# Kernel tuning notes

Measured on AMD Instinct MI355X. Metric: run time of the kernel, lower is better.

The kernel has to match this reference:

```python
import jax, jax.numpy as jnp
import numpy as np

B, T, C, H = 4, 4096, 1024, 64

def setup_inputs() -> dict:
    key = jax.random.key(0)
    kx, kk, kq, kv = jax.random.split(key, 4)
    x = jax.random.normal(kx, (B, T, C), dtype=jnp.float32)
    # causal lower-triangular mask; masked_fill where mask == 0
    mask = jnp.tril(jnp.ones((T, T), dtype=jnp.int32))
    s = 1.0 / np.sqrt(C)
    Wk = jax.random.normal(kk, (H, C), dtype=jnp.float32) * s
    Wq = jax.random.normal(kq, (H, C), dtype=jnp.float32) * s
    Wv = jax.random.normal(kv, (H, C), dtype=jnp.float32) * s
    return {"x": x, "mask": mask, "Wk": Wk, "Wq": Wq, "Wv": Wv}

def reference(x, mask, Wk, Wq, Wv):
    # single-head attention; dropout is identity in eval mode
    scale = Wk.shape[0] ** -0.5  # head_size ** -0.5
    k = jnp.einsum('btc,hc->bth', x, Wk)  # [B,T,H]
    q = jnp.einsum('btc,hc->bth', x, Wq)
    v = jnp.einsum('btc,hc->bth', x, Wv)
    att = jnp.einsum('bqh,bkh->bqk', q, k) * scale  # [B,T,T]
    att = jnp.where(mask == 0, -jnp.inf, att)
    att = jax.nn.softmax(att, axis=-1)
    out = jnp.einsum('bqk,bkh->bqh', att, v)  # [B,T,H]
    return out
```

## Files before the change

### kernel.cpp

```cpp
#include <hip/hip_runtime.h>
#include <hip/hip_bf16.h>

#define BT 16384
#define CDIM 1024
#define HD 64
#define TT 4096

typedef __bf16 bf16x8 __attribute__((ext_vector_type(8)));
typedef __bf16 bf16x4 __attribute__((ext_vector_type(4)));
typedef float f32x4 __attribute__((ext_vector_type(4)));

__device__ __forceinline__ f32x4 mfma16(bf16x8 a, bf16x8 b, f32x4 c){
  return __builtin_amdgcn_mfma_f32_16x16x32_bf16(a, b, c, 0, 0, 0);
}

__global__ __launch_bounds__(256) void wconv_k(const float* __restrict__ Wk,
    const float* __restrict__ Wq, const float* __restrict__ Wv,
    __bf16* __restrict__ Wbf){
  int idx = blockIdx.x*256 + threadIdx.x;
  int e0 = idx*4;
  int n = e0 >> 10;
  int c = e0 & 1023;
  const float* src; float s;
  if (n < 64)      { src = Wk + (size_t)n*CDIM;       s = 1.0f;   }
  else if (n < 128){ src = Wq + (size_t)(n-64)*CDIM;  s = 0.125f; }
  else             { src = Wv + (size_t)(n-128)*CDIM; s = 1.0f;   }
  float4 v = *reinterpret_cast<const float4*>(src + c);
  __bf16* dst = Wbf + e0;
  dst[0]=(__bf16)(v.x*s); dst[1]=(__bf16)(v.y*s);
  dst[2]=(__bf16)(v.z*s); dst[3]=(__bf16)(v.w*s);
}

__global__ __launch_bounds__(512) void proj_k(const float* __restrict__ x,
    const __bf16* __restrict__ Wbf, __bf16* __restrict__ kb,
    __bf16* __restrict__ qb, __bf16* __restrict__ vTb){
  __shared__ __bf16 Wt[192][72];
  __shared__ __bf16 Xt[32][72];

  const int tid  = threadIdx.x;
  const int lane = tid & 63;
  const int w    = tid >> 6;
  const int wr   = w >> 2;
  const int wn   = w & 3;
  const int l15  = lane & 15, g = lane >> 4;
  const long row0 = (long)blockIdx.x*32;

  const int wrw[3] = { tid>>3, (tid+512)>>3, (tid+1024)>>3 };
  const int wc8    = (tid & 7)*8;
  const int xrw = tid >> 4, xc4 = (tid & 15)*4;

  f32x4 acc[3];
  #pragma unroll
  for (int j=0;j<3;j++) acc[j] = (f32x4)(0.0f);

  bf16x8 wreg[3];
  float4 xreg;

  #pragma unroll
  for (int i=0;i<3;i++)
    wreg[i] = *reinterpret_cast<const bf16x8*>(Wbf + (size_t)wrw[i]*CDIM + wc8);
  xreg = *reinterpret_cast<const float4*>(x + (row0 + xrw)*CDIM + xc4);

  for (int kk=0; kk<16; ++kk){
    __syncthreads();
    #pragma unroll
    for (int i=0;i<3;i++)
      *reinterpret_cast<bf16x8*>(&Wt[wrw[i]][wc8]) = wreg[i];
    {
      bf16x4 xv;
      xv[0]=(__bf16)xreg.x; xv[1]=(__bf16)xreg.y;
      xv[2]=(__bf16)xreg.z; xv[3]=(__bf16)xreg.w;
      *reinterpret_cast<bf16x4*>(&Xt[xrw][xc4]) = xv;
    }
    __syncthreads();

    if (kk < 15){
      const int nk0 = (kk+1)*64;
      #pragma unroll
      for (int i=0;i<3;i++)
        wreg[i] = *reinterpret_cast<const bf16x8*>(Wbf + (size_t)wrw[i]*CDIM + nk0 + wc8);
      xreg = *reinterpret_cast<const float4*>(x + (row0 + xrw)*CDIM + nk0 + xc4);
    }

    bf16x8 a0, a1, b0[3], b1[3];
    a0 = *reinterpret_cast<const bf16x8*>(&Xt[wr*16 + l15][g*8]);
    a1 = *reinterpret_cast<const bf16x8*>(&Xt[wr*16 + l15][g*8 + 32]);
    #pragma unroll
    for (int nf=0;nf<3;nf++){
      b0[nf] = *reinterpret_cast<const bf16x8*>(&Wt[wn*48 + nf*16 + l15][g*8]);
      b1[nf] = *reinterpret_cast<const bf16x8*>(&Wt[wn*48 + nf*16 + l15][g*8 + 32]);
    }
    #pragma unroll
    for (int nf=0;nf<3;nf++)
      acc[nf] = mfma16(a1, b1[nf], mfma16(a0, b0[nf], acc[nf]));
  }

  const long bidx = row0 >> 12;
  #pragma unroll
  for (int nf=0;nf<3;nf++){
    const int n0  = wn*48 + nf*16 + l15;
    const int mat = n0 >> 6;
    const int h   = n0 & 63;
    const long rbase = row0 + wr*16 + g*4;
    if (mat == 0){
      #pragma unroll
      for (int r=0;r<4;r++) kb[(rbase+r)*HD + h] = (__bf16)acc[nf][r];
    } else if (mat == 1){
      #pragma unroll
      for (int r=0;r<4;r++) qb[(rbase+r)*HD + h] = (__bf16)acc[nf][r];
    } else {
      bf16x4 t4;
      #pragma unroll
      for (int r=0;r<4;r++) t4[r] = (__bf16)acc[nf][r];
      *reinterpret_cast<bf16x4*>(vTb + (bidx*64 + h)*TT + (rbase & 4095)) = t4;
    }
  }
}

template<int NS>
__global__ __launch_bounds__(256) void attn_part_k(const __bf16* __restrict__ kbg,
    const __bf16* __restrict__ qbg, const __bf16* __restrict__ vT,
    __bf16* __restrict__ po, float* __restrict__ pl){
  __shared__ __bf16 Klds[64][68];
  __shared__ __bf16 Vlds[64][68];
  __shared__ __bf16 Plds[4][16][68];

  const int tid  = threadIdx.x;
  const int lane = tid & 63;
  const int w    = tid >> 6;
  const int l15  = lane & 15, g = lane >> 4;

  const int bi  = blockIdx.x;
  const int b   = bi / (64*NS);
  const int rem = bi % (64*NS);
  const int qt  = 63 - rem / NS;
  const int s   = rem % NS;

  const int ntiles = qt + 1;
  const int lo = ( s      * ntiles) / NS;
  const int hi = ((s + 1) * ntiles) / NS;
  const int pidx = (b*64 + qt)*NS + s;

  if (lo == hi){
    if (l15 == 0){
      #pragma unroll
      for (int r=0;r<4;r++) pl[pidx*64 + w*16 + g*4 + r] = 0.0f;
    }
    return;
  }

  const long qbase = (long)b*TT + (long)qt*64;

  bf16x8 qf0, qf1;
  {
    const __bf16* src = qbg + (qbase + w*16 + l15)*HD + g*8;
    qf0 = *reinterpret_cast<const bf16x8*>(src);
    qf1 = *reinterpret_cast<const bf16x8*>(src + 32);
  }

  f32x4 o[4];
  #pragma unroll
  for (int ch=0; ch<4; ++ch) o[ch] = (f32x4)(0.0f);
  float lp[4] = {0.f, 0.f, 0.f, 0.f};

  const __bf16* vbase = vT + (size_t)b*64*TT;

  const int skey = tid >> 2;
  const int sd0  = (tid & 3) * 16;
  bf16x8 kr0, kr1, vr0, vr1;

  {
    const long kvbase = (long)b*TT + (long)lo*64;
    const __bf16* ks = kbg + (kvbase + skey)*HD + sd0;
    kr0 = *reinterpret_cast<const bf16x8*>(ks);
    kr1 = *reinterpret_cast<const bf16x8*>(ks+8);
    const __bf16* vs = vbase + (size_t)skey*TT + lo*64 + sd0;
    vr0 = *reinterpret_cast<const bf16x8*>(vs);
    vr1 = *reinterpret_cast<const bf16x8*>(vs+8);
  }

  for (int kv=lo; kv<hi; ++kv){
    __syncthreads();
    *reinterpret_cast<bf16x8*>(&Klds[skey][sd0])   = kr0;
    *reinterpret_cast<bf16x8*>(&Klds[skey][sd0+8]) = kr1;
    *reinterpret_cast<bf16x8*>(&Vlds[skey][sd0])   = vr0;
    *reinterpret_cast<bf16x8*>(&Vlds[skey][sd0+8]) = vr1;
    __syncthreads();

    if (kv+1 < hi){
      const long nbase = (long)b*TT + (long)(kv+1)*64;
      const __bf16* ks = kbg + (nbase + skey)*HD + sd0;
      kr0 = *reinterpret_cast<const bf16x8*>(ks);
      kr1 = *reinterpret_cast<const bf16x8*>(ks+8);
      const __bf16* vs = vbase + (size_t)skey*TT + (kv+1)*64 + sd0;
      vr0 = *reinterpret_cast<const bf16x8*>(vs);
      vr1 = *reinterpret_cast<const bf16x8*>(vs+8);
    }

    f32x4 sv[4];
    __builtin_amdgcn_s_setprio(1);
    #pragma unroll
    for (int c=0;c<4;c++){
      bf16x8 kb0 = *reinterpret_cast<const bf16x8*>(&Klds[c*16 + l15][g*8]);
      bf16x8 kb1 = *reinterpret_cast<const bf16x8*>(&Klds[c*16 + l15][g*8 + 32]);
      sv[c] = mfma16(qf0, kb0, (f32x4)(-16.0f));
      sv[c] = mfma16(qf1, kb1, sv[c]);
    }
    __builtin_amdgcn_s_setprio(0);

    if (kv == qt){
      #pragma unroll
      for (int c=0;c<4;c++){
        const int key = c*16 + l15;
        #pragma unroll
        for (int r=0;r<4;r++){
          const int qr = w*16 + g*4 + r;
          if (key > qr) sv[c][r] = -1e30f;
        }
      }
    }

    #pragma unroll
    for (int c=0;c<4;c++){
      #pragma unroll
      for (int r=0;r<4;r++) sv[c][r] = __expf(sv[c][r]);
    }
    #pragma unroll
    for (int r=0;r<4;r++)
      lp[r] += (sv[0][r] + sv[1][r]) + (sv[2][r] + sv[3][r]);

    #pragma unroll
    for (int c=0;c<4;c++){
      #pragma unroll
      for (int r=0;r<4;r++) Plds[w][g*4+r][c*16 + l15] = (__bf16)sv[c][r];
    }
    asm volatile("s_waitcnt lgkmcnt(0)" ::: "memory");
    __builtin_amdgcn_sched_barrier(0);
    bf16x8 pa0 = *reinterpret_cast<const bf16x8*>(&Plds[w][l15][g*8]);
    bf16x8 pa1 = *reinterpret_cast<const bf16x8*>(&Plds[w][l15][g*8 + 32]);

    __builtin_amdgcn_s_setprio(1);
    #pragma unroll
    for (int ch=0; ch<4; ++ch){
      bf16x8 vb0 = *reinterpret_cast<const bf16x8*>(&Vlds[ch*16 + l15][g*8]);
      bf16x8 vb1 = *reinterpret_cast<const bf16x8*>(&Vlds[ch*16 + l15][g*8 + 32]);
      o[ch] = mfma16(pa0, vb0, o[ch]);
      o[ch] = mfma16(pa1, vb1, o[ch]);
    }
    __builtin_amdgcn_s_setprio(0);
  }

  float lr[4];
  #pragma unroll
  for (int r=0;r<4;r++){
    float v = lp[r];
    v += __shfl_xor(v, 1);
    v += __shfl_xor(v, 2);
    v += __shfl_xor(v, 4);
    v += __shfl_xor(v, 8);
    lr[r] = v;
  }
  float rl[4];
  #pragma unroll
  for (int r=0;r<4;r++) rl[r] = (lr[r] > 0.0f) ? 1.0f/lr[r] : 0.0f;

  __bf16* podst = po + (size_t)pidx*4096;
  #pragma unroll
  for (int ch=0; ch<4; ++ch){
    #pragma unroll
    for (int r=0;r<4;r++)
      podst[(w*16 + g*4 + r)*64 + ch*16 + l15] = (__bf16)(o[ch][r] * rl[r]);
  }
  if (l15 == 0){
    #pragma unroll
    for (int r=0;r<4;r++) pl[pidx*64 + w*16 + g*4 + r] = lr[r];
  }
}

template<int NS>
__global__ __launch_bounds__(256) void comb_k(const __bf16* __restrict__ po,
    const float* __restrict__ pl, float* __restrict__ out){
  const int idx   = blockIdx.x*256 + threadIdx.x;
  const int qrow  = idx >> 6;
  const int dim   = idx & 63;
  const int qtg   = qrow >> 6;
  const int rowin = qrow & 63;

  float num = 0.0f, den = 0.0f;
  #pragma unroll
  for (int s=0;s<NS;s++){
    const float l = pl[(qtg*NS + s)*64 + rowin];
    den += l;
    num += l * (float)po[(size_t)(qtg*NS + s)*4096 + rowin*64 + dim];
  }
  out[idx] = num / den;
}

extern "C" void kernel_launch(void* const* d_in, const int* in_sizes, int n_in,
                              void* d_out, int out_size, void* d_ws, size_t ws_size,
                              hipStream_t stream) {
  const float* x  = (const float*)d_in[0];
  const float* Wk = (const float*)d_in[2];
  const float* Wq = (const float*)d_in[3];
  const float* Wv = (const float*)d_in[4];
  float* out = (float*)d_out;

  char* ws = (char*)d_ws;
  __bf16* Wbf = (__bf16*)ws;
  __bf16* kb  = (__bf16*)(ws + 393216);
  __bf16* qb  = (__bf16*)(ws + 2490368);
  __bf16* vTb = (__bf16*)(ws + 4587520);
  __bf16* po  = (__bf16*)(ws + 6684672);

  wconv_k<<<192, 256, 0, stream>>>(Wk, Wq, Wv, Wbf);
  proj_k <<<512, 512, 0, stream>>>(x, Wbf, kb, qb, vTb);

  const size_t need8 = 6684672ull + (size_t)2048*4096*2 + (size_t)2048*64*4;
  if (ws_size >= need8){
    float* pl = (float*)(ws + 6684672 + (size_t)2048*4096*2);
    attn_part_k<8><<<2048, 256, 0, stream>>>(kb, qb, vTb, po, pl);
    comb_k<8>    <<<4096, 256, 0, stream>>>(po, pl, out);
  } else {
    float* pl = (float*)(ws + 6684672 + (size_t)1024*4096*2);
    attn_part_k<4><<<1024, 256, 0, stream>>>(kb, qb, vTb, po, pl);
    comb_k<4>    <<<4096, 256, 0, stream>>>(po, pl, out);
  }
}
```

Measured before the change: 62.84 us.

## Double-buffer LDS tiles in projection kernel with one barrier per step

The projection GEMM now keeps two LDS buffers for the W and x tiles. Global loads run two steps ahead, and each loop iteration has a single barrier where it used to have two. The aim is to cut barrier stalls and overlap global loads and LDS staging with MFMA work. The row padding also changes from 72 to 68 elements, which makes each row 136 bytes. That may misalign 16-byte vector LDS accesses, so they could be split or run slower, and LDS use per block doubles.

New measurement: 60.55 us. 1.04x faster.

```diff
diff --git a/kernel.cpp b/kernel.cpp
--- a/kernel.cpp
+++ b/kernel.cpp
@@ -34,8 +34,8 @@
 __global__ __launch_bounds__(512) void proj_k(const float* __restrict__ x,
     const __bf16* __restrict__ Wbf, __bf16* __restrict__ kb,
     __bf16* __restrict__ qb, __bf16* __restrict__ vTb){
-  __shared__ __bf16 Wt[192][72];
-  __shared__ __bf16 Xt[32][72];
+  __shared__ __bf16 Wt[2][192][68];
+  __shared__ __bf16 Xt[2][32][68];
 
   const int tid  = threadIdx.x;
   const int lane = tid & 63;
@@ -45,54 +45,72 @@
   const int l15  = lane & 15, g = lane >> 4;
   const long row0 = (long)blockIdx.x*32;
 
-  const int wrw[3] = { tid>>3, (tid+512)>>3, (tid+1024)>>3 };
-  const int wc8    = (tid & 7)*8;
-  const int xrw = tid >> 4, xc4 = (tid & 15)*4;
+  const int wrw0 = tid>>3, wrw1 = (tid+512)>>3, wrw2 = (tid+1024)>>3;
+  const int wc8  = (tid & 7)*8;
+  const int xrw  = tid >> 4, xc4 = (tid & 15)*4;
+
+  const float*  xsrc = x + (row0 + xrw)*CDIM + xc4;
+  const __bf16* ws0  = Wbf + (size_t)wrw0*CDIM + wc8;
+  const __bf16* ws1  = Wbf + (size_t)wrw1*CDIM + wc8;
+  const __bf16* ws2  = Wbf + (size_t)wrw2*CDIM + wc8;
 
   f32x4 acc[3];
   #pragma unroll
   for (int j=0;j<3;j++) acc[j] = (f32x4)(0.0f);
 
-  bf16x8 wreg[3];
-  float4 xreg;
-
-  #pragma unroll
-  for (int i=0;i<3;i++)
-    wreg[i] = *reinterpret_cast<const bf16x8*>(Wbf + (size_t)wrw[i]*CDIM + wc8);
-  xreg = *reinterpret_cast<const float4*>(x + (row0 + xrw)*CDIM + xc4);
-
-  for (int kk=0; kk<16; ++kk){
+  bf16x8 w0, w1, w2; float4 xr;
+
+  w0 = *reinterpret_cast<const bf16x8*>(ws0);
+  w1 = *reinterpret_cast<const bf16x8*>(ws1);
+  w2 = *reinterpret_cast<const bf16x8*>(ws2);
+  xr = *reinterpret_cast<const float4*>(xsrc);
+  *reinterpret_cast<bf16x8*>(&Wt[0][wrw0][wc8]) = w0;
+  *reinterpret_cast<bf16x8*>(&Wt[0][wrw1][wc8]) = w1;
+  *reinterpret_cast<bf16x8*>(&Wt[0][wrw2][wc8]) = w2;
+  {
+    bf16x4 xv;
+    xv[0]=(__bf16)xr.x; xv[1]=(__bf16)xr.y; xv[2]=(__bf16)xr.z; xv[3]=(__bf16)xr.w;
+    *reinterpret_cast<bf16x4*>(&Xt[0][xrw][xc4]) = xv;
+  }
+  w0 = *reinterpret_cast<const bf16x8*>(ws0 + 64);
+  w1 = *reinterpret_cast<const bf16x8*>(ws1 + 64);
+  w2 = *reinterpret_cast<const bf16x8*>(ws2 + 64);
+  xr = *reinterpret_cast<const float4*>(xsrc + 64);
+  __syncthreads();
+
+  #pragma unroll 2
+  for (int t=0; t<16; ++t){
+    const int cur = t & 1, nxt = cur ^ 1;
+
+    if (t+1 < 16){
+      *reinterpret_cast<bf16x8*>(&Wt[nxt][wrw0][wc8]) = w0;
+      *reinterpret_cast<bf16x8*>(&Wt[nxt][wrw1][wc8]) = w1;
+      *reinterpret_cast<bf16x8*>(&Wt[nxt][wrw2][wc8]) = w2;
+      bf16x4 xv;
+      xv[0]=(__bf16)xr.x; xv[1]=(__bf16)xr.y; xv[2]=(__bf16)xr.z; xv[3]=(__bf16)xr.w;
+      *reinterpret_cast<bf16x4*>(&Xt[nxt][xrw][xc4]) = xv;
+    }
+    if (t+2 < 16){
+      const int nk0 = (t+2)*64;
+      w0 = *reinterpret_cast<const bf16x8*>(ws0 + nk0);
+      w1 = *reinterpret_cast<const bf16x8*>(ws1 + nk0);
+      w2 = *reinterpret_cast<const bf16x8*>(ws2 + nk0);
+      xr = *reinterpret_cast<const float4*>(xsrc + nk0);
+    }
+    {
+      bf16x8 a0, a1, b0[3], b1[3];
+      a0 = *reinterpret_cast<const bf16x8*>(&Xt[cur][wr*16 + l15][g*8]);
+      a1 = *reinterpret_cast<const bf16x8*>(&Xt[cur][wr*16 + l15][g*8 + 32]);
+      #pragma unroll
+      for (int nf=0;nf<3;nf++){
+        b0[nf] = *reinterpret_cast<const bf16x8*>(&Wt[cur][wn*48 + nf*16 + l15][g*8]);
+        b1[nf] = *reinterpret_cast<const bf16x8*>(&Wt[cur][wn*48 + nf*16 + l15][g*8 + 32]);
+      }
+      #pragma unroll
+      for (int nf=0;nf<3;nf++)
+        acc[nf] = mfma16(a1, b1[nf], mfma16(a0, b0[nf], acc[nf]));
+    }
     __syncthreads();
-    #pragma unroll
-    for (int i=0;i<3;i++)
-      *reinterpret_cast<bf16x8*>(&Wt[wrw[i]][wc8]) = wreg[i];
-    {
-      bf16x4 xv;
-      xv[0]=(__bf16)xreg.x; xv[1]=(__bf16)xreg.y;
-      xv[2]=(__bf16)xreg.z; xv[3]=(__bf16)xreg.w;
-      *reinterpret_cast<bf16x4*>(&Xt[xrw][xc4]) = xv;
-    }
-    __syncthreads();
-
-    if (kk < 15){
-      const int nk0 = (kk+1)*64;
-      #pragma unroll
-      for (int i=0;i<3;i++)
-        wreg[i] = *reinterpret_cast<const bf16x8*>(Wbf + (size_t)wrw[i]*CDIM + nk0 + wc8);
-      xreg = *reinterpret_cast<const float4*>(x + (row0 + xrw)*CDIM + nk0 + xc4);
-    }
-
-    bf16x8 a0, a1, b0[3], b1[3];
-    a0 = *reinterpret_cast<const bf16x8*>(&Xt[wr*16 + l15][g*8]);
-    a1 = *reinterpret_cast<const bf16x8*>(&Xt[wr*16 + l15][g*8 + 32]);
-    #pragma unroll
-    for (int nf=0;nf<3;nf++){
-      b0[nf] = *reinterpret_cast<const bf16x8*>(&Wt[wn*48 + nf*16 + l15][g*8]);
-      b1[nf] = *reinterpret_cast<const bf16x8*>(&Wt[wn*48 + nf*16 + l15][g*8 + 32]);
-    }
-    #pragma unroll
-    for (int nf=0;nf<3;nf++)
-      acc[nf] = mfma16(a1, b1[nf], mfma16(a0, b0[nf], acc[nf]));
   }
 
   const long bidx = row0 >> 12;
```

## Keep projection weights in registers with split-K reduction; vectorize combine kernel

Applied to the files above, without the earlier changes.

The projection kernel now loads each wave's slice of the bf16 weights into registers once and keeps them resident. Each block streams 64 rows of x through a full-width LDS tile in four 16-row chunks, with two wave groups each covering half of the K dimension and summing partials through LDS. This removes the per-step weight reloads and LDS staging of W, at the cost of very high register pressure and fewer blocks (256). The combine kernel processes four output elements per thread with vector loads and stores.

Result: slower. 70.46 us (+12.1%).

```diff
diff --git a/kernel.cpp b/kernel.cpp
--- a/kernel.cpp
+++ b/kernel.cpp
@@ -31,88 +31,90 @@
   dst[2]=(__bf16)(v.z*s); dst[3]=(__bf16)(v.w*s);
 }
 
-__global__ __launch_bounds__(512) void proj_k(const float* __restrict__ x,
+__global__ __launch_bounds__(512, 2) void proj_k(const float* __restrict__ x,
     const __bf16* __restrict__ Wbf, __bf16* __restrict__ kb,
     __bf16* __restrict__ qb, __bf16* __restrict__ vTb){
-  __shared__ __bf16 Wt[192][72];
-  __shared__ __bf16 Xt[32][72];
+  __shared__ __bf16 Xt[16][1032];
+  __shared__ float  redbuf[16][200];
 
   const int tid  = threadIdx.x;
   const int lane = tid & 63;
   const int w    = tid >> 6;
-  const int wr   = w >> 2;
-  const int wn   = w & 3;
+  const int nq   = w & 3;
+  const int kh   = w >> 2;
   const int l15  = lane & 15, g = lane >> 4;
-  const long row0 = (long)blockIdx.x*32;
-
-  const int wrw[3] = { tid>>3, (tid+512)>>3, (tid+1024)>>3 };
-  const int wc8    = (tid & 7)*8;
-  const int xrw = tid >> 4, xc4 = (tid & 15)*4;
-
-  f32x4 acc[3];
-  #pragma unroll
-  for (int j=0;j<3;j++) acc[j] = (f32x4)(0.0f);
-
-  bf16x8 wreg[3];
-  float4 xreg;
-
-  #pragma unroll
-  for (int i=0;i<3;i++)
-    wreg[i] = *reinterpret_cast<const bf16x8*>(Wbf + (size_t)wrw[i]*CDIM + wc8);
-  xreg = *reinterpret_cast<const float4*>(x + (row0 + xrw)*CDIM + xc4);
-
-  for (int kk=0; kk<16; ++kk){
+
+  bf16x8 wf[3][8][2];
+  #pragma unroll
+  for (int f=0; f<3; ++f)
+    #pragma unroll
+    for (int st=0; st<8; ++st)
+      #pragma unroll
+      for (int h=0; h<2; ++h)
+        wf[f][st][h] = *reinterpret_cast<const bf16x8*>(
+            Wbf + (size_t)(nq*48 + f*16 + l15)*CDIM + kh*512 + st*64 + g*8 + h*32);
+
+  const long brow0 = (long)blockIdx.x * 64;
+  const long bidx  = brow0 >> 12;
+
+  for (int mt=0; mt<4; ++mt){
+    const long row0 = brow0 + mt*16;
+
+    #pragma unroll
+    for (int p=0; p<8; ++p){
+      const int i  = p*512 + tid;
+      const int rw = i >> 8, c4 = (i & 255)*4;
+      float4 v = *reinterpret_cast<const float4*>(x + (row0 + rw)*CDIM + c4);
+      bf16x4 xv;
+      xv[0]=(__bf16)v.x; xv[1]=(__bf16)v.y; xv[2]=(__bf16)v.z; xv[3]=(__bf16)v.w;
+      *reinterpret_cast<bf16x4*>(&Xt[rw][c4]) = xv;
+    }
     __syncthreads();
-    #pragma unroll
-    for (int i=0;i<3;i++)
-      *reinterpret_cast<bf16x8*>(&Wt[wrw[i]][wc8]) = wreg[i];
-    {
-      bf16x4 xv;
-      xv[0]=(__bf16)xreg.x; xv[1]=(__bf16)xreg.y;
-      xv[2]=(__bf16)xreg.z; xv[3]=(__bf16)xreg.w;
-      *reinterpret_cast<bf16x4*>(&Xt[xrw][xc4]) = xv;
+
+    f32x4 acc[3];
+    #pragma unroll
+    for (int j=0;j<3;j++) acc[j] = (f32x4)(0.0f);
+    #pragma unroll
+    for (int st=0; st<8; ++st){
+      const int kc = kh*512 + st*64;
+      bf16x8 a0 = *reinterpret_cast<const bf16x8*>(&Xt[l15][kc + g*8]);
+      bf16x8 a1 = *reinterpret_cast<const bf16x8*>(&Xt[l15][kc + g*8 + 32]);
+      #pragma unroll
+      for (int f=0; f<3; ++f)
+        acc[f] = mfma16(a1, wf[f][st][1], mfma16(a0, wf[f][st][0], acc[f]));
+    }
+
+    if (kh == 0){
+      #pragma unroll
+      for (int f=0;f<3;f++)
+        #pragma unroll
+        for (int r=0;r<4;r++)
+          redbuf[g*4 + r][nq*48 + f*16 + l15] = acc[f][r];
     }
     __syncthreads();
-
-    if (kk < 15){
-      const int nk0 = (kk+1)*64;
-      #pragma unroll
-      for (int i=0;i<3;i++)
-        wreg[i] = *reinterpret_cast<const bf16x8*>(Wbf + (size_t)wrw[i]*CDIM + nk0 + wc8);
-      xreg = *reinterpret_cast<const float4*>(x + (row0 + xrw)*CDIM + nk0 + xc4);
-    }
-
-    bf16x8 a0, a1, b0[3], b1[3];
-    a0 = *reinterpret_cast<const bf16x8*>(&Xt[wr*16 + l15][g*8]);
-    a1 = *reinterpret_cast<const bf16x8*>(&Xt[wr*16 + l15][g*8 + 32]);
-    #pragma unroll
-    for (int nf=0;nf<3;nf++){
-      b0[nf] = *reinterpret_cast<const bf16x8*>(&Wt[wn*48 + nf*16 + l15][g*8]);
-      b1[nf] = *reinterpret_cast<const bf16x8*>(&Wt[wn*48 + nf*16 + l15][g*8 + 32]);
-    }
-    #pragma unroll
-    for (int nf=0;nf<3;nf++)
-      acc[nf] = mfma16(a1, b1[nf], mfma16(a0, b0[nf], acc[nf]));
-  }
-
-  const long bidx = row0 >> 12;
-  #pragma unroll
-  for (int nf=0;nf<3;nf++){
-    const int n0  = wn*48 + nf*16 + l15;
-    const int mat = n0 >> 6;
-    const int h   = n0 & 63;
-    const long rbase = row0 + wr*16 + g*4;
-    if (mat == 0){
-      #pragma unroll
-      for (int r=0;r<4;r++) kb[(rbase+r)*HD + h] = (__bf16)acc[nf][r];
-    } else if (mat == 1){
-      #pragma unroll
-      for (int r=0;r<4;r++) qb[(rbase+r)*HD + h] = (__bf16)acc[nf][r];
-    } else {
-      bf16x4 t4;
-      #pragma unroll
-      for (int r=0;r<4;r++) t4[r] = (__bf16)acc[nf][r];
-      *reinterpret_cast<bf16x4*>(vTb + (bidx*64 + h)*TT + (rbase & 4095)) = t4;
+    if (kh == 1){
+      #pragma unroll
+      for (int f=0;f<3;f++){
+        const int n0  = nq*48 + f*16 + l15;
+        const int mat = n0 >> 6;
+        const int h   = n0 & 63;
+        float sum[4];
+        #pragma unroll
+        for (int r=0;r<4;r++) sum[r] = acc[f][r] + redbuf[g*4 + r][n0];
+        const long rbase = row0 + g*4;
+        if (mat == 0){
+          #pragma unroll
+          for (int r=0;r<4;r++) kb[(rbase+r)*HD + h] = (__bf16)sum[r];
+        } else if (mat == 1){
+          #pragma unroll
+          for (int r=0;r<4;r++) qb[(rbase+r)*HD + h] = (__bf16)sum[r];
+        } else {
+          bf16x4 t4;
+          #pragma unroll
+          for (int r=0;r<4;r++) t4[r] = (__bf16)sum[r];
+          *reinterpret_cast<bf16x4*>(vTb + (bidx*64 + h)*TT + (rbase & 4095)) = t4;
+        }
+      }
     }
   }
 }
@@ -280,20 +282,25 @@
 template<int NS>
 __global__ __launch_bounds__(256) void comb_k(const __bf16* __restrict__ po,
     const float* __restrict__ pl, float* __restrict__ out){
-  const int idx   = blockIdx.x*256 + threadIdx.x;
-  const int qrow  = idx >> 6;
-  const int dim   = idx & 63;
+  const int idx4  = (blockIdx.x*256 + threadIdx.x)*4;
+  const int qrow  = idx4 >> 6;
+  const int dim0  = idx4 & 63;
   const int qtg   = qrow >> 6;
   const int rowin = qrow & 63;
 
-  float num = 0.0f, den = 0.0f;
+  float num0=0.f, num1=0.f, num2=0.f, num3=0.f, den=0.f;
   #pragma unroll
   for (int s=0;s<NS;s++){
-    const float l = pl[(qtg*NS + s)*64 + rowin];
-    den += l;
-    num += l * (float)po[(size_t)(qtg*NS + s)*4096 + rowin*64 + dim];
-  }
-  out[idx] = num / den;
+    const float lv = pl[(qtg*NS + s)*64 + rowin];
+    den += lv;
+    bf16x4 p4 = *reinterpret_cast<const bf16x4*>(
+        po + (size_t)(qtg*NS + s)*4096 + rowin*64 + dim0);
+    num0 += lv*(float)p4[0]; num1 += lv*(float)p4[1];
+    num2 += lv*(float)p4[2]; num3 += lv*(float)p4[3];
+  }
+  const float rd = 1.0f/den;
+  float4 o = make_float4(num0*rd, num1*rd, num2*rd, num3*rd);
+  *reinterpret_cast<float4*>(out + idx4) = o;
 }
 
 extern "C" void kernel_launch(void* const* d_in, const int* in_sizes, int n_in,
@@ -313,16 +320,16 @@
   __bf16* po  = (__bf16*)(ws + 6684672);
 
   wconv_k<<<192, 256, 0, stream>>>(Wk, Wq, Wv, Wbf);
-  proj_k <<<512, 512, 0, stream>>>(x, Wbf, kb, qb, vTb);
+  proj_k <<<256, 512, 0, stream>>>(x, Wbf, kb, qb, vTb);
 
   const size_t need8 = 6684672ull + (size_t)2048*4096*2 + (size_t)2048*64*4;
   if (ws_size >= need8){
     float* pl = (float*)(ws + 6684672 + (size_t)2048*4096*2);
     attn_part_k<8><<<2048, 256, 0, stream>>>(kb, qb, vTb, po, pl);
-    comb_k<8>    <<<4096, 256, 0, stream>>>(po, pl, out);
+    comb_k<8>    <<<1024, 256, 0, stream>>>(po, pl, out);
   } else {
     float* pl = (float*)(ws + 6684672 + (size_t)1024*4096*2);
     attn_part_k<4><<<1024, 256, 0, stream>>>(kb, qb, vTb, po, pl);
-    comb_k<4>    <<<4096, 256, 0, stream>>>(po, pl, out);
-  }
-}
+    comb_k<4>    <<<1024, 256, 0, stream>>>(po, pl, out);
+  }
+}
```
